# Kernel tuning notes

Measured on AMD Instinct MI355X. Metric: run time of the kernel, lower is better.

## Reference

```python
import jax, jax.numpy as jnp
import numpy as np

HIDDEN = 1024
N_HEAD = 16
HEAD_DIM = HIDDEN // N_HEAD
ROPE_THETA = 10000.0


def setup_inputs() -> dict:
    key = jax.random.key(0)
    ks = jax.random.split(key, 6)
    B, T = 4, 2048
    x = jax.random.normal(ks[0], (B, T, HIDDEN), dtype=jnp.float32)
    rnn_state = jax.random.normal(ks[1], (B, HIDDEN), dtype=jnp.float32)
    Wqkv = jax.random.normal(ks[2], (HIDDEN, 3 * HIDDEN), dtype=jnp.float32) * 0.02
    bqkv = jnp.zeros((3 * HIDDEN,), dtype=jnp.float32)
    Wproj = jax.random.normal(ks[3], (HIDDEN, HIDDEN), dtype=jnp.float32) * 0.02
    bproj = jnp.zeros((HIDDEN,), dtype=jnp.float32)
    return {"x": x, "rnn_state": rnn_state, "Wqkv": Wqkv, "bqkv": bqkv,
            "Wproj": Wproj, "bproj": bproj}


def _rope_tables(T, dtype):
    # GPT-NeoX style half-split RoPE
    inv_freq = 1.0 / (ROPE_THETA ** (jnp.arange(0, HEAD_DIM, 2, dtype=jnp.float32) / HEAD_DIM))
    freqs = jnp.arange(T, dtype=jnp.float32)[:, None] * inv_freq[None, :]  # [T, D/2]
    return jnp.cos(freqs).astype(dtype), jnp.sin(freqs).astype(dtype)


def _apply_rope(x, cos, sin):
    # x: [B, H, T, D]; cos/sin: [T, D/2]
    x1, x2 = jnp.split(x, 2, axis=-1)
    c = cos[None, None, :, :]
    s = sin[None, None, :, :]
    return jnp.concatenate([x1 * c - x2 * s, x1 * s + x2 * c], axis=-1)


def reference(x, rnn_state, Wqkv, bqkv, Wproj, bproj):
    B, T, C = x.shape
    qkv = x @ Wqkv + bqkv  # [B, T, 3C]
    q, k, v = jnp.split(qkv, 3, axis=-1)
    # split heads -> [B, H, T, D]
    def heads(t):
        return t.reshape(B, T, N_HEAD, HEAD_DIM).transpose(0, 2, 1, 3)
    q, k, v = heads(q), heads(k), heads(v)
    cos, sin = _rope_tables(T, x.dtype)
    q = _apply_rope(q, cos, sin)
    k = _apply_rope(k, cos, sin)
    scale = 1.0 / jnp.sqrt(jnp.asarray(HEAD_DIM, dtype=x.dtype))
    scores = jnp.einsum('bhtd,bhsd->bhts', q, k) * scale  # [B,H,T,T]
    # causal additive mask: 0 on/below diag, -inf above (matches torch buffer)
    causal = jnp.tril(jnp.ones((T, T), dtype=bool))
    scores = jnp.where(causal[None, None, :, :], scores, -jnp.inf)
    attn = jax.nn.softmax(scores, axis=-1)
    out = jnp.einsum('bhts,bhsd->bhtd', attn, v)  # [B,H,T,D]
    out = out.transpose(0, 2, 1, 3).reshape(B, T, C)
    output = out @ Wproj + bproj
    return (output, rnn_state)
```

## Files before the change

### kernel.cpp

```cpp
#include <hip/hip_runtime.h>
#include <cstdint>
#include <cstddef>
#include <math.h>

typedef unsigned short u16;
typedef __attribute__((ext_vector_type(8))) short short8;
typedef __attribute__((ext_vector_type(4))) float floatx4;

#define HIDDEN 1024
#define NHEAD 16
#define HD 64
#define BB 4
#define TT 2048
#define MM (BB*TT)
#define NQKV 3072
#define NEGINF (-30000.0f)

__device__ inline u16 f2bf(float f){
  union { float f; unsigned u; } v; v.f = f;
  unsigned r = v.u + 0x7FFFu + ((v.u >> 16) & 1u);
  return (u16)(r >> 16);
}
__device__ inline void load_lds16(const void* g, void* l){
  __builtin_amdgcn_global_load_lds((const __attribute__((address_space(1))) void*)g,
                                   (__attribute__((address_space(3))) void*)l,
                                   16, 0, 0);
}
__device__ inline short8 cvt8(const float* p){
  const floatx4 a = *(const floatx4*)p;
  const floatx4 b = *(const floatx4*)(p + 4);
  union { short8 s; unsigned u[4]; } r;
  asm("v_cvt_pk_bf16_f32 %0, %1, %2" : "=v"(r.u[0]) : "v"(a[0]), "v"(a[1]));
  asm("v_cvt_pk_bf16_f32 %0, %1, %2" : "=v"(r.u[1]) : "v"(a[2]), "v"(a[3]));
  asm("v_cvt_pk_bf16_f32 %0, %1, %2" : "=v"(r.u[2]) : "v"(b[0]), "v"(b[1]));
  asm("v_cvt_pk_bf16_f32 %0, %1, %2" : "=v"(r.u[3]) : "v"(b[2]), "v"(b[3]));
  return r.s;
}

#define PREP_CONV_BLKS  4096
#define PREP_TQKV_BLKS  (96*32)
#define PREP_TPROJ_BLKS (32*32)
#define PREP_ROPE_BLKS  (TT*32/256)
#define PREP_TAIL_BLKS  ((BB*HIDDEN+255)/256)
#define PREP_BLKS (PREP_CONV_BLKS + PREP_TQKV_BLKS + PREP_TPROJ_BLKS + PREP_ROPE_BLKS + PREP_TAIL_BLKS)

__global__ void prep(const float* __restrict__ x, u16* __restrict__ xN,
                     const float* __restrict__ Wqkv, u16* __restrict__ WqkvT,
                     const float* __restrict__ Wproj, u16* __restrict__ WprojT,
                     float* __restrict__ ropeC, float* __restrict__ ropeS,
                     const float* __restrict__ rnn, float* __restrict__ out)
{
  __shared__ alignas(16) u16 tile[32][33];
  int blk = blockIdx.x;
  const int tid = threadIdx.x;

  if (blk < PREP_CONV_BLKS){
    const int i = (blk * 256 + tid) * 8;
    #pragma unroll
    for (int u = 0; u < 8; u++) xN[i + u] = f2bf(x[i + u]);
    return;
  }
  blk -= PREP_CONV_BLKS;
  if (blk < PREP_TQKV_BLKS + PREP_TPROJ_BLKS){
    const float* in; u16* outp; int R, C, c0, r0;
    if (blk < PREP_TQKV_BLKS){
      in = Wqkv; outp = WqkvT; R = HIDDEN; C = NQKV;
      c0 = (blk % 96) * 32; r0 = (blk / 96) * 32;
    } else {
      const int b2 = blk - PREP_TQKV_BLKS;
      in = Wproj; outp = WprojT; R = HIDDEN; C = HIDDEN;
      c0 = (b2 % 32) * 32; r0 = (b2 / 32) * 32;
    }
    const int tx = tid & 31, ty = tid >> 5;
    for (int i = ty; i < 32; i += 8)
      tile[i][tx] = f2bf(in[(size_t)(r0 + i) * C + c0 + tx]);
    __syncthreads();
    for (int i = ty; i < 32; i += 8) outp[(size_t)(c0 + i) * R + r0 + tx] = tile[tx][i];
    return;
  }
  blk -= PREP_TQKV_BLKS + PREP_TPROJ_BLKS;
  if (blk < PREP_ROPE_BLKS){
    const int idx = blk * 256 + tid;
    const int t = idx >> 5, f = idx & 31;
    const float inv = powf(10000.0f, -(float)f * (1.0f / 32.0f));
    const float ang = (float)t * inv;
    ropeC[idx] = cosf(ang);
    ropeS[idx] = sinf(ang);
    return;
  }
  blk -= PREP_ROPE_BLKS;
  {
    const int i = blk * 256 + tid;
    if (i < BB * HIDDEN) out[(size_t)MM * HIDDEN + i] = rnn[i];
  }
}

__global__ void gemm_qkv(const u16* __restrict__ X, const u16* __restrict__ WT,
                         const float* __restrict__ bias,
                         const float* __restrict__ ropeC, const float* __restrict__ ropeS,
                         u16* __restrict__ Qb, u16* __restrict__ Kb, u16* __restrict__ Vtg)
{
  __shared__ alignas(16) u16 As[128 * 32];
  __shared__ alignas(16) u16 Bs[128 * 32];
  __shared__ alignas(16) u16 VTx[4][64 * 24];
  const int tid = threadIdx.x;
  const int wid = tid >> 6, lane = tid & 63;
  const int quad = lane >> 4, ln = lane & 15;
  const int row0 = blockIdx.y * 128, col0 = blockIdx.x * 128;
  const int wm = (wid >> 1) * 64, wn = (wid & 1) * 64;
  floatx4 acc[4][4] = {};

  const int sr = tid >> 2, sk = (tid & 3) * 8;

  for (int kk = 0; kk < 32; ++kk){
    const int k0 = kk * 32;
    __syncthreads();
    load_lds16(&X [(size_t)(row0 + sr      ) * 1024 + k0 + sk], &As[(size_t)(tid      ) * 8]);
    load_lds16(&X [(size_t)(row0 + sr + 64 ) * 1024 + k0 + sk], &As[(size_t)(tid + 256) * 8]);
    load_lds16(&WT[(size_t)(col0 + sr      ) * 1024 + k0 + sk], &Bs[(size_t)(tid      ) * 8]);
    load_lds16(&WT[(size_t)(col0 + sr + 64 ) * 1024 + k0 + sk], &Bs[(size_t)(tid + 256) * 8]);
    __syncthreads();
    short8 a[4], b[4];
    #pragma unroll
    for (int i = 0; i < 4; i++) a[i] = *(const short8*)&As[(wm + i*16 + ln) * 32 + quad * 8];
    #pragma unroll
    for (int j = 0; j < 4; j++) b[j] = *(const short8*)&Bs[(wn + j*16 + ln) * 32 + quad * 8];
    #pragma unroll
    for (int i = 0; i < 4; i++)
      #pragma unroll
      for (int j = 0; j < 4; j++)
        acc[i][j] = __builtin_amdgcn_mfma_f32_16x16x32_bf16(a[i], b[j], acc[i][j], 0, 0, 0);
  }

  const int wcol0 = col0 + wn;
  const int which = wcol0 >> 10;
  const int h = (wcol0 & 1023) >> 6;
  float bs[4];
  #pragma unroll
  for (int j = 0; j < 4; j++) bs[j] = bias[wcol0 + j*16 + ln];

  if (which < 2){
    #pragma unroll
    for (int i = 0; i < 4; i++){
      #pragma unroll
      for (int rr = 0; rr < 4; rr++){
        const int rowg = row0 + wm + i*16 + quad*4 + rr;
        const int b_ = rowg >> 11, t = rowg & 2047;
        u16* op = (which == 0 ? Qb : Kb) + ((size_t)(b_ * NHEAD + h) * TT + t) * HD;
        #pragma unroll
        for (int j = 0; j < 2; j++){
          const int f = j*16 + ln;
          const float cs = ropeC[t * 32 + f];
          const float sn = ropeS[t * 32 + f];
          const float x1 = acc[i][j  ][rr] + bs[j  ];
          const float x2 = acc[i][j+2][rr] + bs[j+2];
          float y1 = x1 * cs - x2 * sn;
          float y2 = x1 * sn + x2 * cs;
          if (which == 0){ y1 *= 0.125f; y2 *= 0.125f; }
          op[f]      = f2bf(y1);
          op[f + 32] = f2bf(y2);
        }
      }
    }
  } else {
    #pragma unroll
    for (int i = 0; i < 4; i++){
      #pragma unroll
      for (int j = 0; j < 4; j++)
        #pragma unroll
        for (int rr = 0; rr < 4; rr++)
          VTx[wid][(j*16 + ln) * 24 + quad*4 + rr] = f2bf(acc[i][j][rr] + bs[j]);
      asm volatile("s_waitcnt lgkmcnt(0)" ::: "memory");
      const int d = lane;
      const short8 v0 = *(const short8*)&VTx[wid][d * 24 + 0];
      const short8 v1 = *(const short8*)&VTx[wid][d * 24 + 8];
      const int rowg = row0 + wm + i*16;
      const int b_ = rowg >> 11, t0 = rowg & 2047;
      u16* vp = &Vtg[((size_t)(b_ * NHEAD + h) * HD + d) * TT + t0];
      *(short8*)&vp[0] = v0;
      *(short8*)&vp[8] = v1;
      asm volatile("s_waitcnt lgkmcnt(0)" ::: "memory");
    }
  }
}

__global__ void __launch_bounds__(256, 3)
attn(const u16* __restrict__ Qb, const u16* __restrict__ Kb,
     const u16* __restrict__ Vtg, u16* __restrict__ AO)
{
  const int bh = blockIdx.x, tbi = 15 - (int)blockIdx.y;
  const int tid = threadIdx.x;
  const int wid = tid >> 6, lane = tid & 63;
  const int quad = lane >> 4, ln = lane & 15;

  __shared__ alignas(16) u16 Kl2[2][64 * 72];
  __shared__ alignas(16) u16 Vt2[2][64 * 72];
  __shared__ alignas(16) float Plf[4][16 * 68];

  const u16* Qh = Qb  + (size_t)bh * TT * HD;
  const u16* Kh = Kb  + (size_t)bh * TT * HD;
  const u16* Vh = Vtg + (size_t)bh * HD * TT;
  const int b_ = bh >> 4, h = bh & 15;

  const int qbase = tbi * 128 + wid * 32;

  short8 aq[2][2];
  #pragma unroll
  for (int qt = 0; qt < 2; qt++){
    aq[qt][0] = *(const short8*)&Qh[(size_t)(qbase + qt*16 + ln) * HD + quad*8];
    aq[qt][1] = *(const short8*)&Qh[(size_t)(qbase + qt*16 + ln) * HD + 32 + quad*8];
  }

  floatx4 o[2][4] = {};
  float l_i[2][4] = {};
  float* Pf = &Plf[wid][0];

  const int pr = tid >> 3, pc = (tid & 7) * 8;
  short8 kpre0, kpre1, vpre0, vpre1;

  const int nch = 2 * (tbi + 1);

  kpre0 = *(const short8*)&Kh[(size_t)(pr     ) * HD + pc];
  kpre1 = *(const short8*)&Kh[(size_t)(pr + 32) * HD + pc];
  vpre0 = *(const short8*)&Vh[(size_t)(pr     ) * TT + pc];
  vpre1 = *(const short8*)&Vh[(size_t)(pr + 32) * TT + pc];
  *(short8*)&Kl2[0][(pr     ) * 72 + pc] = kpre0;
  *(short8*)&Kl2[0][(pr + 32) * 72 + pc] = kpre1;
  *(short8*)&Vt2[0][(pr     ) * 72 + pc] = vpre0;
  *(short8*)&Vt2[0][(pr + 32) * 72 + pc] = vpre1;
  __syncthreads();

  int cur = 0;
  for (int ch = 0; ch < nch; ++ch){
    const int key0 = ch * 64;
    if (ch + 1 < nch){
      const int nk0 = key0 + 64;
      kpre0 = *(const short8*)&Kh[(size_t)(nk0 + pr     ) * HD + pc];
      kpre1 = *(const short8*)&Kh[(size_t)(nk0 + pr + 32) * HD + pc];
      vpre0 = *(const short8*)&Vh[(size_t)(pr     ) * TT + nk0 + pc];
      vpre1 = *(const short8*)&Vh[(size_t)(pr + 32) * TT + nk0 + pc];
    }

    if (key0 <= qbase + 31){
      const u16* Kl = Kl2[cur];
      const u16* Vt = Vt2[cur];
      const bool act0 = (key0 <= qbase + 15);
      short8 pk0[2], pk1[2];
      #pragma unroll
      for (int qt = 0; qt < 2; qt++){
        if (qt == 0 && !act0) continue;
        const int qt0 = qbase + qt*16;
        floatx4 z[4];
        #pragma unroll
        for (int j = 0; j < 4; j++){
          const short8 kb0 = *(const short8*)&Kl[(j*16 + ln) * 72 + quad*8];
          const short8 kb1 = *(const short8*)&Kl[(j*16 + ln) * 72 + 32 + quad*8];
          floatx4 zz = {0.0f, 0.0f, 0.0f, 0.0f};
          zz = __builtin_amdgcn_mfma_f32_16x16x32_bf16(aq[qt][0], kb0, zz, 0, 0, 0);
          zz = __builtin_amdgcn_mfma_f32_16x16x32_bf16(aq[qt][1], kb1, zz, 0, 0, 0);
          z[j] = zz;
        }
        if (key0 + 63 > qt0){
          #pragma unroll
          for (int j = 0; j < 4; j++)
            #pragma unroll
            for (int rr = 0; rr < 4; rr++){
              const int key = key0 + j*16 + ln;
              const int t   = qt0 + quad*4 + rr;
              if (key > t) z[j][rr] = NEGINF;
            }
        }
        #pragma unroll
        for (int j = 0; j < 4; j++)
          #pragma unroll
          for (int rr = 0; rr < 4; rr++){
            const float p = __expf(z[j][rr]);
            l_i[qt][rr] += p;
            Pf[(quad*4 + rr) * 68 + j*16 + ln] = p;
          }
        asm volatile("s_waitcnt lgkmcnt(0)" ::: "memory");
        pk0[qt] = cvt8(&Pf[ln * 68 + quad*8]);
        pk1[qt] = cvt8(&Pf[ln * 68 + 32 + quad*8]);
      }
      #pragma unroll
      for (int n = 0; n < 4; n++){
        const short8 vb0 = *(const short8*)&Vt[(n*16 + ln) * 72 + quad*8];
        const short8 vb1 = *(const short8*)&Vt[(n*16 + ln) * 72 + 32 + quad*8];
        if (act0){
          o[0][n] = __builtin_amdgcn_mfma_f32_16x16x32_bf16(pk0[0], vb0, o[0][n], 0, 0, 0);
          o[0][n] = __builtin_amdgcn_mfma_f32_16x16x32_bf16(pk1[0], vb1, o[0][n], 0, 0, 0);
        }
        o[1][n] = __builtin_amdgcn_mfma_f32_16x16x32_bf16(pk0[1], vb0, o[1][n], 0, 0, 0);
        o[1][n] = __builtin_amdgcn_mfma_f32_16x16x32_bf16(pk1[1], vb1, o[1][n], 0, 0, 0);
      }
    }

    if (ch + 1 < nch){
      *(short8*)&Kl2[cur ^ 1][(pr     ) * 72 + pc] = kpre0;
      *(short8*)&Kl2[cur ^ 1][(pr + 32) * 72 + pc] = kpre1;
      *(short8*)&Vt2[cur ^ 1][(pr     ) * 72 + pc] = vpre0;
      *(short8*)&Vt2[cur ^ 1][(pr + 32) * 72 + pc] = vpre1;
    }
    __syncthreads();
    cur ^= 1;
  }

  #pragma unroll
  for (int qt = 0; qt < 2; qt++)
    #pragma unroll
    for (int rr = 0; rr < 4; rr++){
      float rs = l_i[qt][rr];
      #pragma unroll
      for (int off = 1; off < 16; off <<= 1) rs += __shfl_xor(rs, off);
      l_i[qt][rr] = rs;
    }

  #pragma unroll
  for (int qt = 0; qt < 2; qt++)
    #pragma unroll
    for (int n = 0; n < 4; n++)
      #pragma unroll
      for (int rr = 0; rr < 4; rr++){
        const int t = qbase + qt*16 + quad*4 + rr;
        const float inv_l = 1.0f / fmaxf(l_i[qt][rr], 1e-20f);
        AO[(size_t)(b_ * TT + t) * HIDDEN + h * HD + n*16 + ln] = f2bf(o[qt][n][rr] * inv_l);
      }
}

__global__ void gemm_proj(const u16* __restrict__ A, const u16* __restrict__ WT,
                          const float* __restrict__ bias, float* __restrict__ out)
{
  __shared__ alignas(16) u16 As[128 * 32];
  __shared__ alignas(16) u16 Bs[128 * 32];
  const int tid = threadIdx.x;
  const int wid = tid >> 6, lane = tid & 63;
  const int quad = lane >> 4, ln = lane & 15;
  const int row0 = blockIdx.y * 128, col0 = blockIdx.x * 128;
  const int wm = (wid >> 1) * 64, wn = (wid & 1) * 64;
  floatx4 acc[4][4] = {};

  const int sr = tid >> 2, sk = (tid & 3) * 8;

  for (int kk = 0; kk < 32; ++kk){
    const int k0 = kk * 32;
    __syncthreads();
    load_lds16(&A [(size_t)(row0 + sr      ) * 1024 + k0 + sk], &As[(size_t)(tid      ) * 8]);
    load_lds16(&A [(size_t)(row0 + sr + 64 ) * 1024 + k0 + sk], &As[(size_t)(tid + 256) * 8]);
    load_lds16(&WT[(size_t)(col0 + sr      ) * 1024 + k0 + sk], &Bs[(size_t)(tid      ) * 8]);
    load_lds16(&WT[(size_t)(col0 + sr + 64 ) * 1024 + k0 + sk], &Bs[(size_t)(tid + 256) * 8]);
    __syncthreads();
    short8 a[4], b[4];
    #pragma unroll
    for (int i = 0; i < 4; i++) a[i] = *(const short8*)&As[(wm + i*16 + ln) * 32 + quad * 8];
    #pragma unroll
    for (int j = 0; j < 4; j++) b[j] = *(const short8*)&Bs[(wn + j*16 + ln) * 32 + quad * 8];
    #pragma unroll
    for (int i = 0; i < 4; i++)
      #pragma unroll
      for (int j = 0; j < 4; j++)
        acc[i][j] = __builtin_amdgcn_mfma_f32_16x16x32_bf16(a[i], b[j], acc[i][j], 0, 0, 0);
  }

  float bs[4];
  #pragma unroll
  for (int j = 0; j < 4; j++) bs[j] = bias[col0 + wn + j*16 + ln];
  #pragma unroll
  for (int i = 0; i < 4; i++)
    #pragma unroll
    for (int rr = 0; rr < 4; rr++){
      const int rowg = row0 + wm + i*16 + quad*4 + rr;
      #pragma unroll
      for (int j = 0; j < 4; j++)
        out[(size_t)rowg * HIDDEN + col0 + wn + j*16 + ln] = acc[i][j][rr] + bs[j];
    }
}

extern "C" void kernel_launch(void* const* d_in, const int* in_sizes, int n_in,
                              void* d_out, int out_size, void* d_ws, size_t ws_size,
                              hipStream_t stream)
{
  const float* x     = (const float*)d_in[0];
  const float* rnn   = (const float*)d_in[1];
  const float* Wqkv  = (const float*)d_in[2];
  const float* bqkv  = (const float*)d_in[3];
  const float* Wproj = (const float*)d_in[4];
  const float* bproj = (const float*)d_in[5];
  float* out = (float*)d_out;

  char* ws = (char*)d_ws;
  size_t off = 0;
  float* ropeC  = (float*)(ws + off); off += (size_t)TT * 32 * 4;
  float* ropeS  = (float*)(ws + off); off += (size_t)TT * 32 * 4;
  u16*   xN     = (u16*)(ws + off);   off += (size_t)MM * HIDDEN * 2;
  u16*   WqkvT  = (u16*)(ws + off);   off += (size_t)NQKV * HIDDEN * 2;
  u16*   WprojT = (u16*)(ws + off);   off += (size_t)HIDDEN * HIDDEN * 2;
  u16*   Qb     = (u16*)(ws + off);   off += (size_t)MM * HIDDEN * 2;
  u16*   Kb     = (u16*)(ws + off);   off += (size_t)MM * HIDDEN * 2;
  u16*   Vtg    = (u16*)(ws + off);   off += (size_t)MM * HIDDEN * 2;
  u16*   AO     = (u16*)(ws + off);   off += (size_t)MM * HIDDEN * 2;

  prep<<<PREP_BLKS, 256, 0, stream>>>(x, xN, Wqkv, WqkvT, Wproj, WprojT,
                                      ropeC, ropeS, rnn, out);
  gemm_qkv<<<dim3(NQKV / 128, MM / 128), 256, 0, stream>>>(xN, WqkvT, bqkv, ropeC, ropeS, Qb, Kb, Vtg);
  attn<<<dim3(BB * NHEAD, 16), 256, 0, stream>>>(Qb, Kb, Vtg, AO);
  gemm_proj<<<dim3(HIDDEN / 128, MM / 128), 256, 0, stream>>>(AO, WprojT, bproj, out);
}
```

Before: 264.6 us.

## Load K/V fragments directly from global memory in attention, dropping LDS staging

The attention kernel no longer stages K and V tiles in double-buffered shared memory with block-wide barriers. Each wave now reads its MFMA operand fragments straight from global memory (relying on L1/L2 reuse) and runs only as many key chunks as its own causal range needs. Launch bounds are raised to target 4 blocks per CU now that LDS usage is smaller. The trade-off is more global/cache traffic, since the four waves each fetch the same K/V, and less latency hiding, because there is no prefetch.

```diff
diff --git a/kernel.cpp b/kernel.cpp
--- a/kernel.cpp
+++ b/kernel.cpp
@@ -184,7 +184,7 @@
   }
 }
 
-__global__ void __launch_bounds__(256, 3)
+__global__ void __launch_bounds__(256, 4)
 attn(const u16* __restrict__ Qb, const u16* __restrict__ Kb,
      const u16* __restrict__ Vtg, u16* __restrict__ AO)
 {
@@ -193,8 +193,6 @@
   const int wid = tid >> 6, lane = tid & 63;
   const int quad = lane >> 4, ln = lane & 15;
 
-  __shared__ alignas(16) u16 Kl2[2][64 * 72];
-  __shared__ alignas(16) u16 Vt2[2][64 * 72];
   __shared__ alignas(16) float Plf[4][16 * 68];
 
   const u16* Qh = Qb  + (size_t)bh * TT * HD;
@@ -215,94 +213,63 @@
   float l_i[2][4] = {};
   float* Pf = &Plf[wid][0];
 
-  const int pr = tid >> 3, pc = (tid & 7) * 8;
-  short8 kpre0, kpre1, vpre0, vpre1;
-
-  const int nch = 2 * (tbi + 1);
-
-  kpre0 = *(const short8*)&Kh[(size_t)(pr     ) * HD + pc];
-  kpre1 = *(const short8*)&Kh[(size_t)(pr + 32) * HD + pc];
-  vpre0 = *(const short8*)&Vh[(size_t)(pr     ) * TT + pc];
-  vpre1 = *(const short8*)&Vh[(size_t)(pr + 32) * TT + pc];
-  *(short8*)&Kl2[0][(pr     ) * 72 + pc] = kpre0;
-  *(short8*)&Kl2[0][(pr + 32) * 72 + pc] = kpre1;
-  *(short8*)&Vt2[0][(pr     ) * 72 + pc] = vpre0;
-  *(short8*)&Vt2[0][(pr + 32) * 72 + pc] = vpre1;
-  __syncthreads();
-
-  int cur = 0;
-  for (int ch = 0; ch < nch; ++ch){
+  const u16* Krow = Kh + (size_t)ln * HD + quad * 8;
+  const u16* Vrow = Vh + (size_t)ln * TT + quad * 8;
+
+  const int nch_w = ((qbase + 31) >> 6) + 1;
+  for (int ch = 0; ch < nch_w; ++ch){
     const int key0 = ch * 64;
-    if (ch + 1 < nch){
-      const int nk0 = key0 + 64;
-      kpre0 = *(const short8*)&Kh[(size_t)(nk0 + pr     ) * HD + pc];
-      kpre1 = *(const short8*)&Kh[(size_t)(nk0 + pr + 32) * HD + pc];
-      vpre0 = *(const short8*)&Vh[(size_t)(pr     ) * TT + nk0 + pc];
-      vpre1 = *(const short8*)&Vh[(size_t)(pr + 32) * TT + nk0 + pc];
-    }
-
-    if (key0 <= qbase + 31){
-      const u16* Kl = Kl2[cur];
-      const u16* Vt = Vt2[cur];
-      const bool act0 = (key0 <= qbase + 15);
-      short8 pk0[2], pk1[2];
-      #pragma unroll
-      for (int qt = 0; qt < 2; qt++){
-        if (qt == 0 && !act0) continue;
-        const int qt0 = qbase + qt*16;
-        floatx4 z[4];
-        #pragma unroll
-        for (int j = 0; j < 4; j++){
-          const short8 kb0 = *(const short8*)&Kl[(j*16 + ln) * 72 + quad*8];
-          const short8 kb1 = *(const short8*)&Kl[(j*16 + ln) * 72 + 32 + quad*8];
-          floatx4 zz = {0.0f, 0.0f, 0.0f, 0.0f};
-          zz = __builtin_amdgcn_mfma_f32_16x16x32_bf16(aq[qt][0], kb0, zz, 0, 0, 0);
-          zz = __builtin_amdgcn_mfma_f32_16x16x32_bf16(aq[qt][1], kb1, zz, 0, 0, 0);
-          z[j] = zz;
-        }
-        if (key0 + 63 > qt0){
-          #pragma unroll
-          for (int j = 0; j < 4; j++)
-            #pragma unroll
-            for (int rr = 0; rr < 4; rr++){
-              const int key = key0 + j*16 + ln;
-              const int t   = qt0 + quad*4 + rr;
-              if (key > t) z[j][rr] = NEGINF;
-            }
-        }
+    const bool act0 = (key0 <= qbase + 15);
+    short8 pk0[2], pk1[2];
+    #pragma unroll
+    for (int qt = 0; qt < 2; qt++){
+      if (qt == 0 && !act0) continue;
+      const int qt0 = qbase + qt*16;
+      floatx4 z[4];
+      #pragma unroll
+      for (int j = 0; j < 4; j++){
+        const u16* kp = Krow + (size_t)(key0 + j*16) * HD;
+        const short8 kb0 = *(const short8*)kp;
+        const short8 kb1 = *(const short8*)(kp + 32);
+        floatx4 zz = {0.0f, 0.0f, 0.0f, 0.0f};
+        zz = __builtin_amdgcn_mfma_f32_16x16x32_bf16(aq[qt][0], kb0, zz, 0, 0, 0);
+        zz = __builtin_amdgcn_mfma_f32_16x16x32_bf16(aq[qt][1], kb1, zz, 0, 0, 0);
+        z[j] = zz;
+      }
+      if (key0 + 63 > qt0){
         #pragma unroll
         for (int j = 0; j < 4; j++)
           #pragma unroll
           for (int rr = 0; rr < 4; rr++){
-            const float p = __expf(z[j][rr]);
-            l_i[qt][rr] += p;
-            Pf[(quad*4 + rr) * 68 + j*16 + ln] = p;
+            const int key = key0 + j*16 + ln;
+            const int t   = qt0 + quad*4 + rr;
+            if (key > t) z[j][rr] = NEGINF;
           }
-        asm volatile("s_waitcnt lgkmcnt(0)" ::: "memory");
-        pk0[qt] = cvt8(&Pf[ln * 68 + quad*8]);
-        pk1[qt] = cvt8(&Pf[ln * 68 + 32 + quad*8]);
-      }
-      #pragma unroll
-      for (int n = 0; n < 4; n++){
-        const short8 vb0 = *(const short8*)&Vt[(n*16 + ln) * 72 + quad*8];
-        const short8 vb1 = *(const short8*)&Vt[(n*16 + ln) * 72 + 32 + quad*8];
-        if (act0){
-          o[0][n] = __builtin_amdgcn_mfma_f32_16x16x32_bf16(pk0[0], vb0, o[0][n], 0, 0, 0);
-          o[0][n] = __builtin_amdgcn_mfma_f32_16x16x32_bf16(pk1[0], vb1, o[0][n], 0, 0, 0);
+      }
+      #pragma unroll
+      for (int j = 0; j < 4; j++)
+        #pragma unroll
+        for (int rr = 0; rr < 4; rr++){
+          const float p = __expf(z[j][rr]);
+          l_i[qt][rr] += p;
+          Pf[(quad*4 + rr) * 68 + j*16 + ln] = p;
         }
-        o[1][n] = __builtin_amdgcn_mfma_f32_16x16x32_bf16(pk0[1], vb0, o[1][n], 0, 0, 0);
-        o[1][n] = __builtin_amdgcn_mfma_f32_16x16x32_bf16(pk1[1], vb1, o[1][n], 0, 0, 0);
-      }
-    }
-
-    if (ch + 1 < nch){
-      *(short8*)&Kl2[cur ^ 1][(pr     ) * 72 + pc] = kpre0;
-      *(short8*)&Kl2[cur ^ 1][(pr + 32) * 72 + pc] = kpre1;
-      *(short8*)&Vt2[cur ^ 1][(pr     ) * 72 + pc] = vpre0;
-      *(short8*)&Vt2[cur ^ 1][(pr + 32) * 72 + pc] = vpre1;
-    }
-    __syncthreads();
-    cur ^= 1;
+      asm volatile("s_waitcnt lgkmcnt(0)" ::: "memory");
+      pk0[qt] = cvt8(&Pf[ln * 68 + quad*8]);
+      pk1[qt] = cvt8(&Pf[ln * 68 + 32 + quad*8]);
+    }
+    #pragma unroll
+    for (int n = 0; n < 4; n++){
+      const u16* vp = Vrow + (size_t)(n*16) * TT + key0;
+      const short8 vb0 = *(const short8*)vp;
+      const short8 vb1 = *(const short8*)(vp + 32);
+      if (act0){
+        o[0][n] = __builtin_amdgcn_mfma_f32_16x16x32_bf16(pk0[0], vb0, o[0][n], 0, 0, 0);
+        o[0][n] = __builtin_amdgcn_mfma_f32_16x16x32_bf16(pk1[0], vb1, o[0][n], 0, 0, 0);
+      }
+      o[1][n] = __builtin_amdgcn_mfma_f32_16x16x32_bf16(pk0[1], vb0, o[1][n], 0, 0, 0);
+      o[1][n] = __builtin_amdgcn_mfma_f32_16x16x32_bf16(pk1[1], vb1, o[1][n], 0, 0, 0);
+    }
   }
 
   #pragma unroll
```

Result: slower. 410.3 us (+55.0%).

## Double-buffer QKV GEMM with 256x128 tiles, BK=64 and swizzled LDS

Applied to the files above, without the earlier changes.

Rewrites the QKV projection GEMM main loop to use 512-thread blocks covering 256x128 output tiles with a K-step of 64. Global-to-LDS loads are double-buffered so the next stage is in flight while MFMAs run on the current one. An XOR swizzle on LDS columns is meant to cut bank conflicts. This removes the per-iteration load/compute serialization of the old single-buffer loop, at the cost of more LDS per block (about 100KB) and lower block-level occupancy.

```diff
diff --git a/kernel.cpp b/kernel.cpp
--- a/kernel.cpp
+++ b/kernel.cpp
@@ -15,6 +15,7 @@
 #define MM (BB*TT)
 #define NQKV 3072
 #define NEGINF (-30000.0f)
+#define GFENCE() asm volatile("" ::: "memory")
 
 __device__ inline u16 f2bf(float f){
   union { float f; unsigned u; } v; v.f = f;
@@ -95,41 +96,83 @@
   }
 }
 
-__global__ void gemm_qkv(const u16* __restrict__ X, const u16* __restrict__ WT,
-                         const float* __restrict__ bias,
-                         const float* __restrict__ ropeC, const float* __restrict__ ropeS,
-                         u16* __restrict__ Qb, u16* __restrict__ Kb, u16* __restrict__ Vtg)
+__global__ void __launch_bounds__(512, 2)
+gemm_qkv(const u16* __restrict__ X, const u16* __restrict__ WT,
+         const float* __restrict__ bias,
+         const float* __restrict__ ropeC, const float* __restrict__ ropeS,
+         u16* __restrict__ Qb, u16* __restrict__ Kb, u16* __restrict__ Vtg)
 {
-  __shared__ alignas(16) u16 As[128 * 32];
-  __shared__ alignas(16) u16 Bs[128 * 32];
-  __shared__ alignas(16) u16 VTx[4][64 * 24];
+  __shared__ alignas(16) u16 As[2][256 * 64];
+  __shared__ alignas(16) u16 Bs[2][128 * 64];
+  __shared__ alignas(16) u16 VTx[8][64 * 24];
   const int tid = threadIdx.x;
   const int wid = tid >> 6, lane = tid & 63;
   const int quad = lane >> 4, ln = lane & 15;
-  const int row0 = blockIdx.y * 128, col0 = blockIdx.x * 128;
+  const int row0 = blockIdx.y * 256, col0 = blockIdx.x * 128;
   const int wm = (wid >> 1) * 64, wn = (wid & 1) * 64;
   floatx4 acc[4][4] = {};
 
-  const int sr = tid >> 2, sk = (tid & 3) * 8;
-
-  for (int kk = 0; kk < 32; ++kk){
-    const int k0 = kk * 32;
-    __syncthreads();
-    load_lds16(&X [(size_t)(row0 + sr      ) * 1024 + k0 + sk], &As[(size_t)(tid      ) * 8]);
-    load_lds16(&X [(size_t)(row0 + sr + 64 ) * 1024 + k0 + sk], &As[(size_t)(tid + 256) * 8]);
-    load_lds16(&WT[(size_t)(col0 + sr      ) * 1024 + k0 + sk], &Bs[(size_t)(tid      ) * 8]);
-    load_lds16(&WT[(size_t)(col0 + sr + 64 ) * 1024 + k0 + sk], &Bs[(size_t)(tid + 256) * 8]);
-    __syncthreads();
-    short8 a[4], b[4];
-    #pragma unroll
-    for (int i = 0; i < 4; i++) a[i] = *(const short8*)&As[(wm + i*16 + ln) * 32 + quad * 8];
-    #pragma unroll
-    for (int j = 0; j < 4; j++) b[j] = *(const short8*)&Bs[(wn + j*16 + ln) * 32 + quad * 8];
-    #pragma unroll
-    for (int i = 0; i < 4; i++)
-      #pragma unroll
-      for (int j = 0; j < 4; j++)
-        acc[i][j] = __builtin_amdgcn_mfma_f32_16x16x32_bf16(a[i], b[j], acc[i][j], 0, 0, 0);
+#define QSTAGE(buf, t) do {                                                                  \
+    const int k0_ = (t) * 64;                                                                \
+    _Pragma("unroll")                                                                        \
+    for (int i_ = 0; i_ < 4; i_++){                                                          \
+      const int idx_ = i_ * 512 + tid; const int r_ = idx_ >> 3, c8_ = idx_ & 7;             \
+      load_lds16(&X[(size_t)(row0 + r_) * 1024 + k0_ + ((c8_*8) ^ ((r_&3)<<4))],             \
+                 &As[buf][(size_t)idx_ * 8]);                                                \
+    }                                                                                        \
+    _Pragma("unroll")                                                                        \
+    for (int i_ = 0; i_ < 2; i_++){                                                          \
+      const int idx_ = i_ * 512 + tid; const int r_ = idx_ >> 3, c8_ = idx_ & 7;             \
+      load_lds16(&WT[(size_t)(col0 + r_) * 1024 + k0_ + ((c8_*8) ^ ((r_&3)<<4))],            \
+                 &Bs[buf][(size_t)idx_ * 8]);                                                \
+    }                                                                                        \
+  } while (0)
+
+#define QCOMPUTE(buf) do {                                                                   \
+    short8 b0[4], b1[4];                                                                     \
+    _Pragma("unroll")                                                                        \
+    for (int n = 0; n < 4; n++){                                                             \
+      const int br = wn + n*16 + ln; const int sw = (br & 3) << 4;                           \
+      b0[n] = *(const short8*)&Bs[buf][br*64 + ((quad*8) ^ sw)];                             \
+      b1[n] = *(const short8*)&Bs[buf][br*64 + ((32 + quad*8) ^ sw)];                        \
+    }                                                                                        \
+    _Pragma("unroll")                                                                        \
+    for (int m = 0; m < 4; m++){                                                             \
+      const int ar = wm + m*16 + ln; const int sw = (ar & 3) << 4;                           \
+      const short8 a0 = *(const short8*)&As[buf][ar*64 + ((quad*8) ^ sw)];                   \
+      const short8 a1 = *(const short8*)&As[buf][ar*64 + ((32 + quad*8) ^ sw)];              \
+      _Pragma("unroll")                                                                      \
+      for (int n = 0; n < 4; n++){                                                           \
+        acc[m][n] = __builtin_amdgcn_mfma_f32_16x16x32_bf16(a0, b0[n], acc[m][n], 0, 0, 0);  \
+        acc[m][n] = __builtin_amdgcn_mfma_f32_16x16x32_bf16(a1, b1[n], acc[m][n], 0, 0, 0);  \
+      }                                                                                      \
+    }                                                                                        \
+  } while (0)
+
+  QSTAGE(0, 0);
+  QSTAGE(1, 1);
+  asm volatile("s_waitcnt vmcnt(6)" ::: "memory");
+  __builtin_amdgcn_s_barrier();
+  GFENCE();
+
+  #pragma unroll 2
+  for (int t = 0; t < 16; ++t){
+    const int cur = t & 1;
+    QCOMPUTE(cur);
+    GFENCE();
+    asm volatile("s_waitcnt lgkmcnt(0)" ::: "memory");
+    __builtin_amdgcn_s_barrier();
+    GFENCE();
+    if (t < 14){
+      QSTAGE(cur, t + 2);
+      asm volatile("s_waitcnt vmcnt(6)" ::: "memory");
+      __builtin_amdgcn_s_barrier();
+      GFENCE();
+    } else if (t == 14){
+      asm volatile("s_waitcnt vmcnt(0)" ::: "memory");
+      __builtin_amdgcn_s_barrier();
+      GFENCE();
+    }
   }
 
   const int wcol0 = col0 + wn;
@@ -141,10 +184,10 @@
 
   if (which < 2){
     #pragma unroll
-    for (int i = 0; i < 4; i++){
+    for (int m = 0; m < 4; m++){
       #pragma unroll
       for (int rr = 0; rr < 4; rr++){
-        const int rowg = row0 + wm + i*16 + quad*4 + rr;
+        const int rowg = row0 + wm + m*16 + quad*4 + rr;
         const int b_ = rowg >> 11, t = rowg & 2047;
         u16* op = (which == 0 ? Qb : Kb) + ((size_t)(b_ * NHEAD + h) * TT + t) * HD;
         #pragma unroll
@@ -152,8 +195,8 @@
           const int f = j*16 + ln;
           const float cs = ropeC[t * 32 + f];
           const float sn = ropeS[t * 32 + f];
-          const float x1 = acc[i][j  ][rr] + bs[j  ];
-          const float x2 = acc[i][j+2][rr] + bs[j+2];
+          const float x1 = acc[m][j  ][rr] + bs[j  ];
+          const float x2 = acc[m][j+2][rr] + bs[j+2];
           float y1 = x1 * cs - x2 * sn;
           float y2 = x1 * sn + x2 * cs;
           if (which == 0){ y1 *= 0.125f; y2 *= 0.125f; }
@@ -164,17 +207,17 @@
     }
   } else {
     #pragma unroll
-    for (int i = 0; i < 4; i++){
+    for (int m = 0; m < 4; m++){
       #pragma unroll
       for (int j = 0; j < 4; j++)
         #pragma unroll
         for (int rr = 0; rr < 4; rr++)
-          VTx[wid][(j*16 + ln) * 24 + quad*4 + rr] = f2bf(acc[i][j][rr] + bs[j]);
+          VTx[wid][(j*16 + ln) * 24 + quad*4 + rr] = f2bf(acc[m][j][rr] + bs[j]);
       asm volatile("s_waitcnt lgkmcnt(0)" ::: "memory");
       const int d = lane;
       const short8 v0 = *(const short8*)&VTx[wid][d * 24 + 0];
       const short8 v1 = *(const short8*)&VTx[wid][d * 24 + 8];
-      const int rowg = row0 + wm + i*16;
+      const int rowg = row0 + wm + m*16;
       const int b_ = rowg >> 11, t0 = rowg & 2047;
       u16* vp = &Vtg[((size_t)(b_ * NHEAD + h) * HD + d) * TT + t0];
       *(short8*)&vp[0] = v0;
@@ -182,6 +225,8 @@
       asm volatile("s_waitcnt lgkmcnt(0)" ::: "memory");
     }
   }
+#undef QSTAGE
+#undef QCOMPUTE
 }
 
 __global__ void __launch_bounds__(256, 3)
@@ -401,7 +446,7 @@
 
   prep<<<PREP_BLKS, 256, 0, stream>>>(x, xN, Wqkv, WqkvT, Wproj, WprojT,
                                       ropeC, ropeS, rnn, out);
-  gemm_qkv<<<dim3(NQKV / 128, MM / 128), 256, 0, stream>>>(xN, WqkvT, bqkv, ropeC, ropeS, Qb, Kb, Vtg);
+  gemm_qkv<<<dim3(NQKV / 128, MM / 256), 512, 0, stream>>>(xN, WqkvT, bqkv, ropeC, ropeS, Qb, Kb, Vtg);
   attn<<<dim3(BB * NHEAD, 16), 256, 0, stream>>>(Qb, Kb, Vtg, AO);
   gemm_proj<<<dim3(HIDDEN / 128, MM / 128), 256, 0, stream>>>(AO, WprojT, bproj, out);
 }
```

New measurement: 270.5 us. 1.02x slower.
